# Kernel optimization log

Hardware: AMD Instinct MI355X
Metric: run time of the kernel (lower is better)

Reference implementation:

```python
import jax, jax.numpy as jnp
import numpy as np

EPS = 1e-12  # torch F.normalize eps

def _l2norm(x):
    n = jnp.linalg.norm(x, axis=-1, keepdims=True)
    return x / jnp.maximum(n, EPS)

def _encode(h, mask, W, b):
    # h: [B,S,H], mask: [B,S] int
    h = h * mask[..., None].astype(h.dtype)      # zero padded tokens
    pooled = h[:, 0]                             # pooling_type='cls'
    col = h[:, 1:] @ W + b                       # colbert_linear on tokens 1:
    return _l2norm(pooled), _l2norm(col)         # normalize=True


def setup_inputs() -> dict:
    key = jax.random.key(0)
    k1, k2, k3, k4, k5, k6 = jax.random.split(key, 6)
    Q, Sq, C, Sc, H, D = 64, 32, 256, 256, 768, 128
    return {
        "q_hidden": jax.random.normal(k1, (Q, Sq, H), jnp.float32),
        "c_hidden": jax.random.normal(k2, (C, Sc, H), jnp.float32),
        "W": jax.random.normal(k3, (H, D), jnp.float32) / np.sqrt(H).astype(np.float32),
        "b": jax.random.normal(k4, (D,), jnp.float32) * 0.01,
        "q_mask": jax.random.randint(k5, (Q, Sq), 0, 2, jnp.int32),
        "c_mask": jax.random.randint(k6, (C, Sc), 0, 2, jnp.int32),
    }


def reference(q_hidden, c_hidden, W, b, q_mask, c_mask):
    q_pooled, q_col = _encode(q_hidden, q_mask, W, b)   # q_col: [Q, Sq-1, D]
    c_pooled, c_col = _encode(c_hidden, c_mask, W, b)   # c_col: [C, Sc-1, D]
    # MaxSim late interaction (get_batch_colbert_sim)
    token_sim = jnp.einsum('qin,cjn->qicj', q_col, c_col)  # [Q, Sq-1, C, Sc-1]
    sim = token_sim.max(axis=-1)                           # max over doc tokens j
    denom = q_mask[:, 1:].sum(-1, keepdims=True).astype(sim.dtype)
    sim = sim.sum(axis=1) / denom                          # [Q, C]
    return sim, q_pooled, c_pooled
```

## Files before the change

### kernel.cpp

```cpp
#include <hip/hip_runtime.h>
#include <hip/hip_bf16.h>

#define QN 64
#define SQ 32
#define CN 256
#define SC 256
#define HD 768
#define DD 128

typedef __attribute__((ext_vector_type(8))) short short8;
typedef __attribute__((ext_vector_type(4))) float f32x4;

static __device__ __forceinline__ unsigned short f2bf(float x) {
  unsigned u = __float_as_uint(x);
  unsigned r = 0x7FFFu + ((u >> 16) & 1u);
  return (unsigned short)((u + r) >> 16);
}
static __device__ __forceinline__ unsigned pack2(float a, float b) {
  return (unsigned)f2bf(a) | ((unsigned)f2bf(b) << 16);
}

typedef const __attribute__((address_space(1))) unsigned int* as1_u32p;
typedef __attribute__((address_space(3))) unsigned int* as3_u32p;
static __device__ __forceinline__ void gl_lds16(const void* g, void* l) {
  __builtin_amdgcn_global_load_lds((as1_u32p)g, (as3_u32p)l, 16, 0, 0);
}

__global__ __launch_bounds__(256) void prep_kernel(
    const float* __restrict__ W,
    const float* __restrict__ qh, const int* __restrict__ qm,
    const float* __restrict__ ch, const int* __restrict__ cm,
    unsigned short* __restrict__ WtS,
    float* __restrict__ outq, float* __restrict__ outc,
    unsigned short* __restrict__ qcolP) {
  __shared__ float red[4];
  int bid = blockIdx.x, tid = threadIdx.x;

  if (bid < DD) {
    int d = bid;
    if (tid < 96) {
      int kc = tid;
      unsigned p[4];
#pragma unroll
      for (int e = 0; e < 4; ++e) {
        float a = W[(size_t)(kc * 8 + 2 * e) * DD + d];
        float b = W[(size_t)(kc * 8 + 2 * e + 1) * DD + d];
        p[e] = pack2(a, b);
      }
      int kcp = (kc & ~7) | ((kc & 7) ^ (d & 7));
      *(uint4*)&WtS[((size_t)d * 96 + kcp) * 8] = *(uint4*)p;
    }
    return;
  }

  int row = bid - DD;
  const float* src;
  float* dst;
  float m;
  if (row < QN) {
    src = qh + (size_t)row * SQ * HD;
    m = (float)qm[row * SQ];
    dst = outq + (size_t)row * HD;
  } else {
    int b = row - QN;
    src = ch + (size_t)b * SC * HD;
    m = (float)cm[b * SC];
    dst = outc + (size_t)b * HD;
  }
  float ss = 0.f;
  for (int k = tid; k < HD; k += 256) {
    float v = src[k] * m;
    ss += v * v;
  }
  int lane = tid & 63, wv = tid >> 6;
  for (int off = 32; off; off >>= 1) ss += __shfl_xor(ss, off);
  if (lane == 0) red[wv] = ss;
  __syncthreads();
  float tot = red[0] + red[1] + red[2] + red[3];
  float inv = 1.f / fmaxf(sqrtf(tot), 1e-12f);
  for (int k = tid; k < HD; k += 256) dst[k] = src[k] * m * inv;
  if (row < QN && tid < 64)
    ((unsigned*)(qcolP + ((size_t)row * 32 + 31) * DD))[tid] = 0u;
}

union ProjLDS {
  struct { float a[128 * 64]; unsigned short w[128 * 64]; } s;
  float cep[64 * 132];
};

__global__ __launch_bounds__(256, 3) void proj_kernel(
    const float* __restrict__ q_hidden, const float* __restrict__ c_hidden,
    const int* __restrict__ q_mask, const int* __restrict__ c_mask,
    const unsigned short* __restrict__ WtS, const float* __restrict__ bias,
    unsigned short* __restrict__ qcol, unsigned short* __restrict__ ccol) {
  __shared__ ProjLDS u;
  int bx = blockIdx.x;
  int isQ = (bx >= 510) ? 1 : 0;
  int base = isQ ? (bx - 510) : bx;
  int tid = threadIdx.x, lane = tid & 63, wv = tid >> 6;
  int lm = lane & 15, lq = lane >> 4;

  int ac = (tid & 8) | ((tid & 7) ^ ((tid >> 4) & 7));
  const float* aptr[8];
#pragma unroll
  for (int i = 0; i < 8; ++i) {
    int r = i * 16 + (tid >> 4);
    int g = base * 128 + r;
    const float* hp;
    if (isQ) {
      g = (g < 1983) ? g : 1983;
      int qq = g / 31, t = g - qq * 31;
      hp = q_hidden + ((size_t)qq * SQ + t + 1) * HD;
    } else {
      int cb = g / 255, t = g - cb * 255;
      hp = c_hidden + ((size_t)cb * SC + t + 1) * HD;
    }
    aptr[i] = hp + ac * 4;
  }
  const unsigned short* wptr[4];
#pragma unroll
  for (int i = 0; i < 4; ++i) {
    int d = i * 32 + (tid >> 3);
    wptr[i] = WtS + ((size_t)d * 96 + (tid & 7)) * 8;
  }

  f32x4 acc[2][8];
#pragma unroll
  for (int i = 0; i < 2; ++i)
#pragma unroll
    for (int j = 0; j < 8; ++j) acc[i][j] = (f32x4){0.f, 0.f, 0.f, 0.f};

  for (int step = 0; step < 12; ++step) {
    __syncthreads();
#pragma unroll
    for (int i = 0; i < 8; ++i)
      gl_lds16(aptr[i] + step * 64, (char*)u.s.a + (size_t)(i * 256 + wv * 64) * 16);
#pragma unroll
    for (int i = 0; i < 4; ++i)
      gl_lds16(wptr[i] + step * 64, (char*)u.s.w + (size_t)(i * 256 + wv * 64) * 16);
    __syncthreads();

#pragma unroll
    for (int w = 0; w < 2; ++w) {
      short8 afr[2];
#pragma unroll
      for (int mt = 0; mt < 2; ++mt) {
        int rr = wv * 32 + mt * 16 + lm;
        int x0 = (lq * 2) ^ (lm & 7);
        int x1 = (lq * 2 + 1) ^ (lm & 7);
        float4 a0 = *(const float4*)&u.s.a[rr * 64 + w * 32 + x0 * 4];
        float4 a1 = *(const float4*)&u.s.a[rr * 64 + w * 32 + x1 * 4];
        unsigned p[4];
        p[0] = pack2(a0.x, a0.y); p[1] = pack2(a0.z, a0.w);
        p[2] = pack2(a1.x, a1.y); p[3] = pack2(a1.z, a1.w);
        afr[mt] = *(short8*)p;
      }
      short8 bfr[8];
#pragma unroll
      for (int nt = 0; nt < 8; ++nt) {
        int d = nt * 16 + lm;
        int pc = (w * 4 + lq) ^ (lm & 7);
        bfr[nt] = *(const short8*)&u.s.w[d * 64 + pc * 8];
      }
#pragma unroll
      for (int mt = 0; mt < 2; ++mt)
#pragma unroll
        for (int nt = 0; nt < 8; ++nt)
          acc[mt][nt] = __builtin_amdgcn_mfma_f32_16x16x32_bf16(afr[mt], bfr[nt], acc[mt][nt], 0, 0, 0);
    }
  }

  int tk = tid >> 2, qt = tid & 3;
#pragma unroll
  for (int h = 0; h < 2; ++h) {
    __syncthreads();
    if ((wv >> 1) == h) {
#pragma unroll
      for (int mt = 0; mt < 2; ++mt)
#pragma unroll
        for (int nt = 0; nt < 8; ++nt)
#pragma unroll
          for (int r = 0; r < 4; ++r) {
            int row = (wv & 1) * 32 + mt * 16 + lq * 4 + r;
            u.cep[row * 132 + nt * 16 + lm] = acc[mt][nt][r];
          }
    }
    __syncthreads();

    int g = base * 128 + h * 64 + tk;
    int qq, t, valid = 1;
    float fm;
    if (isQ) {
      if (g > 1983) { valid = 0; g = 1983; }
      qq = g / 31; t = g - qq * 31;
      fm = (float)q_mask[qq * SQ + t + 1];
    } else {
      qq = g / 255; t = g - qq * 255;
      fm = (float)c_mask[qq * SC + t + 1];
    }

    float v[32];
    float ss = 0.f;
#pragma unroll
    for (int j = 0; j < 8; ++j) {
      float4 cv = *(const float4*)&u.cep[tk * 132 + qt * 32 + j * 4];
      float4 bv = *(const float4*)&bias[qt * 32 + j * 4];
      v[4 * j + 0] = cv.x * fm + bv.x; v[4 * j + 1] = cv.y * fm + bv.y;
      v[4 * j + 2] = cv.z * fm + bv.z; v[4 * j + 3] = cv.w * fm + bv.w;
#pragma unroll
      for (int e = 0; e < 4; ++e) ss += v[4 * j + e] * v[4 * j + e];
    }
    ss += __shfl_xor(ss, 1);
    ss += __shfl_xor(ss, 2);
    float inv = 1.f / fmaxf(sqrtf(ss), 1e-12f);

    uint4 pk4[4];
#pragma unroll
    for (int j = 0; j < 4; ++j) {
      unsigned p[4];
#pragma unroll
      for (int e = 0; e < 4; ++e)
        p[e] = pack2(v[8 * j + 2 * e] * inv, v[8 * j + 2 * e + 1] * inv);
      pk4[j] = *(uint4*)p;
    }

    if (isQ) {
      if (valid) {
        uint4* dst = (uint4*)(qcol + ((size_t)qq * 32 + t) * DD + qt * 32);
#pragma unroll
        for (int j = 0; j < 4; ++j) dst[j] = pk4[j];
      }
    } else {
      uint4* rowp = (uint4*)(ccol + ((size_t)qq * 256 + t) * DD);
#pragma unroll
      for (int j = 0; j < 4; ++j) {
        int kc = qt * 4 + j;
        int p = (kc & 8) | ((kc & 7) ^ (t & 7));
        rowp[p] = pk4[j];
      }
      if (t == 254) {
        uint4* rowp2 = rowp + 8;
#pragma unroll
        for (int j = 0; j < 4; ++j) {
          int kc = qt * 4 + j;
          int p = (kc & 8) | ((kc & 7) ^ 7);
          rowp2[p] = pk4[j];
        }
      }
    }
  }
}

__global__ __launch_bounds__(256, 2) void sim_kernel(
    const unsigned short* __restrict__ qcolP,
    const unsigned short* __restrict__ ccol,
    const int* __restrict__ qmask,
    float* __restrict__ sim) {
  __shared__ unsigned short cbuf[256 * 128];
  int tid = threadIdx.x, lane = tid & 63, wv = tid >> 6;
  int lm = lane & 15, lq = lane >> 4;
  int qb = blockIdx.y * 16 + wv * 4;
  int c0 = blockIdx.x * 2;

  short8 af[4][2][4];
#pragma unroll
  for (int q2 = 0; q2 < 4; ++q2)
#pragma unroll
    for (int it = 0; it < 2; ++it)
#pragma unroll
      for (int kf = 0; kf < 4; ++kf)
        af[q2][it][kf] = *(const short8*)(qcolP +
            (((size_t)(qb + q2) * 32 + it * 16 + lm) * DD + kf * 32 + lq * 8));

  float dinv[4];
#pragma unroll
  for (int q2 = 0; q2 < 4; ++q2) {
    float v = (lane >= 1 && lane < 32) ? (float)qmask[(qb + q2) * SQ + lane] : 0.f;
    for (int off = 1; off < 64; off <<= 1) v += __shfl_xor(v, off);
    dinv[q2] = 1.f / v;
  }

  for (int cc = 0; cc < 2; ++cc) {
    int c = c0 + cc;
    __syncthreads();
    const unsigned short* src = ccol + (size_t)c * SC * DD;
#pragma unroll
    for (int i = 0; i < 16; ++i)
      gl_lds16(src + (size_t)(i * 256 + wv * 64 + lane) * 8,
               (char*)cbuf + (size_t)(i * 256 + wv * 64) * 16);
    __syncthreads();

    float rmax[4][2];
#pragma unroll
    for (int q2 = 0; q2 < 4; ++q2) { rmax[q2][0] = -__builtin_inff(); rmax[q2][1] = -__builtin_inff(); }

    for (int jt = 0; jt < 16; ++jt) {
      short8 cf[4];
#pragma unroll
      for (int kf = 0; kf < 4; ++kf) {
        int row = jt * 16 + lm;
        int kc = kf * 4 + lq;
        int p = (kc & 8) | ((kc & 7) ^ (row & 7));
        cf[kf] = *(const short8*)&cbuf[(size_t)(row * 16 + p) * 8];
      }
#pragma unroll
      for (int q2 = 0; q2 < 4; ++q2)
#pragma unroll
        for (int it = 0; it < 2; ++it) {
          f32x4 acc = (f32x4){0.f, 0.f, 0.f, 0.f};
#pragma unroll
          for (int kf = 0; kf < 4; ++kf)
            acc = __builtin_amdgcn_mfma_f32_16x16x32_bf16(cf[kf], af[q2][it][kf], acc, 0, 0, 0);
          float loc = fmaxf(fmaxf(acc[0], acc[1]), fmaxf(acc[2], acc[3]));
          rmax[q2][it] = fmaxf(rmax[q2][it], loc);
        }
    }

#pragma unroll
    for (int q2 = 0; q2 < 4; ++q2) {
      float m0 = rmax[q2][0], m1 = rmax[q2][1];
      m0 = fmaxf(m0, __shfl_xor(m0, 16)); m0 = fmaxf(m0, __shfl_xor(m0, 32));
      m1 = fmaxf(m1, __shfl_xor(m1, 16)); m1 = fmaxf(m1, __shfl_xor(m1, 32));
      float s = m0 + ((lm == 15) ? 0.f : m1);
      s += __shfl_xor(s, 1); s += __shfl_xor(s, 2);
      s += __shfl_xor(s, 4); s += __shfl_xor(s, 8);
      if (lane == 0) sim[(qb + q2) * CN + c] = s * dinv[q2];
    }
  }
}

extern "C" void kernel_launch(void* const* d_in, const int* in_sizes, int n_in,
                              void* d_out, int out_size, void* d_ws, size_t ws_size,
                              hipStream_t stream) {
  const float* q_hidden = (const float*)d_in[0];
  const float* c_hidden = (const float*)d_in[1];
  const float* W = (const float*)d_in[2];
  const float* bias = (const float*)d_in[3];
  const int* q_mask = (const int*)d_in[4];
  const int* c_mask = (const int*)d_in[5];

  float* out = (float*)d_out;
  float* sim = out;
  float* q_pooled = out + QN * CN;
  float* c_pooled = q_pooled + QN * HD;

  unsigned short* WtS   = (unsigned short*)d_ws;
  unsigned short* qcolP = (unsigned short*)((char*)d_ws + (256 << 10));
  unsigned short* ccol  = (unsigned short*)((char*)d_ws + (1 << 20));

  prep_kernel<<<DD + QN + CN, 256, 0, stream>>>(W, q_hidden, q_mask, c_hidden, c_mask,
                                                WtS, q_pooled, c_pooled, qcolP);
  proj_kernel<<<526, 256, 0, stream>>>(q_hidden, c_hidden, q_mask, c_mask,
                                       WtS, bias, qcolP, ccol);
  sim_kernel<<<dim3(128, 4), 256, 0, stream>>>(qcolP, ccol, q_mask, sim);
}
```

Measured before the change: 362.9 us.

## Double-buffer LDS loads in projection and MaxSim kernels, halve projection tile

The projection kernel now works on 64-row tiles instead of 128-row tiles, so twice as many blocks are launched. Its K loop double-buffers the activation and weight tiles in LDS, loading the next step while MFMAs run on the current one. The MaxSim kernel splits each document's 256 tokens into two 128-row halves, also double-buffered, so global-to-LDS copies overlap compute. The projection change costs lower per-block register reuse (one M tile per wave) and occupancy drops to 2 blocks per SIMD. The pad-row write for token 255 is also corrected to land at the true next row.

```diff
diff --git a/kernel.cpp b/kernel.cpp
--- a/kernel.cpp
+++ b/kernel.cpp
@@ -84,31 +84,30 @@
 }
 
 union ProjLDS {
-  struct { float a[128 * 64]; unsigned short w[128 * 64]; } s;
+  struct { float a[2][64 * 64]; unsigned short w[2][128 * 64]; } s;
   float cep[64 * 132];
 };
 
-__global__ __launch_bounds__(256, 3) void proj_kernel(
+__global__ __launch_bounds__(256, 2) void proj_kernel(
     const float* __restrict__ q_hidden, const float* __restrict__ c_hidden,
     const int* __restrict__ q_mask, const int* __restrict__ c_mask,
     const unsigned short* __restrict__ WtS, const float* __restrict__ bias,
     unsigned short* __restrict__ qcol, unsigned short* __restrict__ ccol) {
   __shared__ ProjLDS u;
   int bx = blockIdx.x;
-  int isQ = (bx >= 510) ? 1 : 0;
-  int base = isQ ? (bx - 510) : bx;
+  int isQ = (bx >= 1020) ? 1 : 0;
+  int base = isQ ? (bx - 1020) : bx;
   int tid = threadIdx.x, lane = tid & 63, wv = tid >> 6;
   int lm = lane & 15, lq = lane >> 4;
 
   int ac = (tid & 8) | ((tid & 7) ^ ((tid >> 4) & 7));
-  const float* aptr[8];
-#pragma unroll
-  for (int i = 0; i < 8; ++i) {
+  const float* aptr[4];
+#pragma unroll
+  for (int i = 0; i < 4; ++i) {
     int r = i * 16 + (tid >> 4);
-    int g = base * 128 + r;
+    int g = base * 64 + r;
     const float* hp;
     if (isQ) {
-      g = (g < 1983) ? g : 1983;
       int qq = g / 31, t = g - qq * 31;
       hp = q_hidden + ((size_t)qq * SQ + t + 1) * HD;
     } else {
@@ -124,128 +123,118 @@
     wptr[i] = WtS + ((size_t)d * 96 + (tid & 7)) * 8;
   }
 
-  f32x4 acc[2][8];
-#pragma unroll
-  for (int i = 0; i < 2; ++i)
-#pragma unroll
-    for (int j = 0; j < 8; ++j) acc[i][j] = (f32x4){0.f, 0.f, 0.f, 0.f};
+  f32x4 acc[8];
+#pragma unroll
+  for (int j = 0; j < 8; ++j) acc[j] = (f32x4){0.f, 0.f, 0.f, 0.f};
+
+#pragma unroll
+  for (int i = 0; i < 4; ++i)
+    gl_lds16(aptr[i], (char*)&u.s.a[0][0] + (size_t)(i * 256 + wv * 64) * 16);
+#pragma unroll
+  for (int i = 0; i < 4; ++i)
+    gl_lds16(wptr[i], (char*)&u.s.w[0][0] + (size_t)(i * 256 + wv * 64) * 16);
+  __syncthreads();
 
   for (int step = 0; step < 12; ++step) {
-    __syncthreads();
-#pragma unroll
-    for (int i = 0; i < 8; ++i)
-      gl_lds16(aptr[i] + step * 64, (char*)u.s.a + (size_t)(i * 256 + wv * 64) * 16);
-#pragma unroll
-    for (int i = 0; i < 4; ++i)
-      gl_lds16(wptr[i] + step * 64, (char*)u.s.w + (size_t)(i * 256 + wv * 64) * 16);
-    __syncthreads();
-
+    int cur = step & 1;
+    if (step < 11) {
+      int nxt = cur ^ 1;
+#pragma unroll
+      for (int i = 0; i < 4; ++i)
+        gl_lds16(aptr[i] + (step + 1) * 64,
+                 (char*)&u.s.a[nxt][0] + (size_t)(i * 256 + wv * 64) * 16);
+#pragma unroll
+      for (int i = 0; i < 4; ++i)
+        gl_lds16(wptr[i] + (step + 1) * 64,
+                 (char*)&u.s.w[nxt][0] + (size_t)(i * 256 + wv * 64) * 16);
+    }
 #pragma unroll
     for (int w = 0; w < 2; ++w) {
-      short8 afr[2];
-#pragma unroll
-      for (int mt = 0; mt < 2; ++mt) {
-        int rr = wv * 32 + mt * 16 + lm;
-        int x0 = (lq * 2) ^ (lm & 7);
-        int x1 = (lq * 2 + 1) ^ (lm & 7);
-        float4 a0 = *(const float4*)&u.s.a[rr * 64 + w * 32 + x0 * 4];
-        float4 a1 = *(const float4*)&u.s.a[rr * 64 + w * 32 + x1 * 4];
-        unsigned p[4];
-        p[0] = pack2(a0.x, a0.y); p[1] = pack2(a0.z, a0.w);
-        p[2] = pack2(a1.x, a1.y); p[3] = pack2(a1.z, a1.w);
-        afr[mt] = *(short8*)p;
-      }
-      short8 bfr[8];
+      int rr = wv * 16 + lm;
+      int x0 = (lq * 2) ^ (lm & 7);
+      int x1 = (lq * 2 + 1) ^ (lm & 7);
+      float4 a0 = *(const float4*)&u.s.a[cur][rr * 64 + w * 32 + x0 * 4];
+      float4 a1 = *(const float4*)&u.s.a[cur][rr * 64 + w * 32 + x1 * 4];
+      unsigned p[4];
+      p[0] = pack2(a0.x, a0.y); p[1] = pack2(a0.z, a0.w);
+      p[2] = pack2(a1.x, a1.y); p[3] = pack2(a1.z, a1.w);
+      short8 afr = *(short8*)p;
 #pragma unroll
       for (int nt = 0; nt < 8; ++nt) {
         int d = nt * 16 + lm;
         int pc = (w * 4 + lq) ^ (lm & 7);
-        bfr[nt] = *(const short8*)&u.s.w[d * 64 + pc * 8];
-      }
-#pragma unroll
-      for (int mt = 0; mt < 2; ++mt)
-#pragma unroll
-        for (int nt = 0; nt < 8; ++nt)
-          acc[mt][nt] = __builtin_amdgcn_mfma_f32_16x16x32_bf16(afr[mt], bfr[nt], acc[mt][nt], 0, 0, 0);
-    }
-  }
+        short8 bfr = *(const short8*)&u.s.w[cur][d * 64 + pc * 8];
+        acc[nt] = __builtin_amdgcn_mfma_f32_16x16x32_bf16(afr, bfr, acc[nt], 0, 0, 0);
+      }
+    }
+    __syncthreads();
+  }
+
+#pragma unroll
+  for (int nt = 0; nt < 8; ++nt)
+#pragma unroll
+    for (int r = 0; r < 4; ++r) {
+      int row = wv * 16 + lq * 4 + r;
+      u.cep[row * 132 + nt * 16 + lm] = acc[nt][r];
+    }
+  __syncthreads();
 
   int tk = tid >> 2, qt = tid & 3;
-#pragma unroll
-  for (int h = 0; h < 2; ++h) {
-    __syncthreads();
-    if ((wv >> 1) == h) {
-#pragma unroll
-      for (int mt = 0; mt < 2; ++mt)
-#pragma unroll
-        for (int nt = 0; nt < 8; ++nt)
-#pragma unroll
-          for (int r = 0; r < 4; ++r) {
-            int row = (wv & 1) * 32 + mt * 16 + lq * 4 + r;
-            u.cep[row * 132 + nt * 16 + lm] = acc[mt][nt][r];
-          }
-    }
-    __syncthreads();
-
-    int g = base * 128 + h * 64 + tk;
-    int qq, t, valid = 1;
-    float fm;
-    if (isQ) {
-      if (g > 1983) { valid = 0; g = 1983; }
-      qq = g / 31; t = g - qq * 31;
-      fm = (float)q_mask[qq * SQ + t + 1];
-    } else {
-      qq = g / 255; t = g - qq * 255;
-      fm = (float)c_mask[qq * SC + t + 1];
-    }
-
-    float v[32];
-    float ss = 0.f;
-#pragma unroll
-    for (int j = 0; j < 8; ++j) {
-      float4 cv = *(const float4*)&u.cep[tk * 132 + qt * 32 + j * 4];
-      float4 bv = *(const float4*)&bias[qt * 32 + j * 4];
-      v[4 * j + 0] = cv.x * fm + bv.x; v[4 * j + 1] = cv.y * fm + bv.y;
-      v[4 * j + 2] = cv.z * fm + bv.z; v[4 * j + 3] = cv.w * fm + bv.w;
-#pragma unroll
-      for (int e = 0; e < 4; ++e) ss += v[4 * j + e] * v[4 * j + e];
-    }
-    ss += __shfl_xor(ss, 1);
-    ss += __shfl_xor(ss, 2);
-    float inv = 1.f / fmaxf(sqrtf(ss), 1e-12f);
-
-    uint4 pk4[4];
+  int g = base * 64 + tk;
+  int qq, t;
+  float fm;
+  if (isQ) {
+    qq = g / 31; t = g - qq * 31;
+    fm = (float)q_mask[qq * SQ + t + 1];
+  } else {
+    qq = g / 255; t = g - qq * 255;
+    fm = (float)c_mask[qq * SC + t + 1];
+  }
+
+  float v[32];
+  float ss = 0.f;
+#pragma unroll
+  for (int j = 0; j < 8; ++j) {
+    float4 cv = *(const float4*)&u.cep[tk * 132 + qt * 32 + j * 4];
+    float4 bv = *(const float4*)&bias[qt * 32 + j * 4];
+    v[4 * j + 0] = cv.x * fm + bv.x; v[4 * j + 1] = cv.y * fm + bv.y;
+    v[4 * j + 2] = cv.z * fm + bv.z; v[4 * j + 3] = cv.w * fm + bv.w;
+#pragma unroll
+    for (int e = 0; e < 4; ++e) ss += v[4 * j + e] * v[4 * j + e];
+  }
+  ss += __shfl_xor(ss, 1);
+  ss += __shfl_xor(ss, 2);
+  float inv = 1.f / fmaxf(sqrtf(ss), 1e-12f);
+
+  uint4 pk4[4];
+#pragma unroll
+  for (int j = 0; j < 4; ++j) {
+    unsigned p[4];
+#pragma unroll
+    for (int e = 0; e < 4; ++e)
+      p[e] = pack2(v[8 * j + 2 * e] * inv, v[8 * j + 2 * e + 1] * inv);
+    pk4[j] = *(uint4*)p;
+  }
+
+  if (isQ) {
+    uint4* dst = (uint4*)(qcol + ((size_t)qq * 32 + t) * DD + qt * 32);
+#pragma unroll
+    for (int j = 0; j < 4; ++j) dst[j] = pk4[j];
+  } else {
+    uint4* rowp = (uint4*)(ccol + ((size_t)qq * 256 + t) * DD);
 #pragma unroll
     for (int j = 0; j < 4; ++j) {
-      unsigned p[4];
-#pragma unroll
-      for (int e = 0; e < 4; ++e)
-        p[e] = pack2(v[8 * j + 2 * e] * inv, v[8 * j + 2 * e + 1] * inv);
-      pk4[j] = *(uint4*)p;
-    }
-
-    if (isQ) {
-      if (valid) {
-        uint4* dst = (uint4*)(qcol + ((size_t)qq * 32 + t) * DD + qt * 32);
-#pragma unroll
-        for (int j = 0; j < 4; ++j) dst[j] = pk4[j];
-      }
-    } else {
-      uint4* rowp = (uint4*)(ccol + ((size_t)qq * 256 + t) * DD);
+      int kc = qt * 4 + j;
+      int p = (kc & 8) | ((kc & 7) ^ (t & 7));
+      rowp[p] = pk4[j];
+    }
+    if (t == 254) {
+      uint4* rowp2 = rowp + 16;
 #pragma unroll
       for (int j = 0; j < 4; ++j) {
         int kc = qt * 4 + j;
-        int p = (kc & 8) | ((kc & 7) ^ (t & 7));
-        rowp[p] = pk4[j];
-      }
-      if (t == 254) {
-        uint4* rowp2 = rowp + 8;
-#pragma unroll
-        for (int j = 0; j < 4; ++j) {
-          int kc = qt * 4 + j;
-          int p = (kc & 8) | ((kc & 7) ^ 7);
-          rowp2[p] = pk4[j];
-        }
+        int p = (kc & 8) | ((kc & 7) ^ 7);
+        rowp2[p] = pk4[j];
       }
     }
   }
@@ -256,7 +245,7 @@
     const unsigned short* __restrict__ ccol,
     const int* __restrict__ qmask,
     float* __restrict__ sim) {
-  __shared__ unsigned short cbuf[256 * 128];
+  __shared__ unsigned short cbuf[2][128 * 128];
   int tid = threadIdx.x, lane = tid & 63, wv = tid >> 6;
   int lm = lane & 15, lq = lane >> 4;
   int qb = blockIdx.y * 16 + wv * 4;
@@ -280,28 +269,40 @@
     dinv[q2] = 1.f / v;
   }
 
-  for (int cc = 0; cc < 2; ++cc) {
-    int c = c0 + cc;
-    __syncthreads();
-    const unsigned short* src = ccol + (size_t)c * SC * DD;
-#pragma unroll
-    for (int i = 0; i < 16; ++i)
-      gl_lds16(src + (size_t)(i * 256 + wv * 64 + lane) * 8,
-               (char*)cbuf + (size_t)(i * 256 + wv * 64) * 16);
-    __syncthreads();
-
-    float rmax[4][2];
-#pragma unroll
-    for (int q2 = 0; q2 < 4; ++q2) { rmax[q2][0] = -__builtin_inff(); rmax[q2][1] = -__builtin_inff(); }
-
-    for (int jt = 0; jt < 16; ++jt) {
+  const unsigned short* csrc = ccol + (size_t)c0 * SC * DD;
+
+#pragma unroll
+  for (int i = 0; i < 8; ++i)
+    gl_lds16(csrc + (size_t)(i * 256 + tid) * 8,
+             (char*)&cbuf[0][0] + (size_t)(i * 256 + wv * 64) * 16);
+  __syncthreads();
+
+  float rmax[4][2];
+  for (int ht = 0; ht < 4; ++ht) {
+    int b = ht & 1;
+    if (!(ht & 1)) {
+#pragma unroll
+      for (int q2 = 0; q2 < 4; ++q2) {
+        rmax[q2][0] = -__builtin_inff();
+        rmax[q2][1] = -__builtin_inff();
+      }
+    }
+    if (ht < 3) {
+      const unsigned short* s2 = csrc + (size_t)(ht + 1) * 16384;
+#pragma unroll
+      for (int i = 0; i < 8; ++i)
+        gl_lds16(s2 + (size_t)(i * 256 + tid) * 8,
+                 (char*)&cbuf[b ^ 1][0] + (size_t)(i * 256 + wv * 64) * 16);
+    }
+
+    for (int jt = 0; jt < 8; ++jt) {
       short8 cf[4];
 #pragma unroll
       for (int kf = 0; kf < 4; ++kf) {
         int row = jt * 16 + lm;
         int kc = kf * 4 + lq;
         int p = (kc & 8) | ((kc & 7) ^ (row & 7));
-        cf[kf] = *(const short8*)&cbuf[(size_t)(row * 16 + p) * 8];
+        cf[kf] = *(const short8*)&cbuf[b][(size_t)(row * 16 + p) * 8];
       }
 #pragma unroll
       for (int q2 = 0; q2 < 4; ++q2)
@@ -316,16 +317,20 @@
         }
     }
 
-#pragma unroll
-    for (int q2 = 0; q2 < 4; ++q2) {
-      float m0 = rmax[q2][0], m1 = rmax[q2][1];
-      m0 = fmaxf(m0, __shfl_xor(m0, 16)); m0 = fmaxf(m0, __shfl_xor(m0, 32));
-      m1 = fmaxf(m1, __shfl_xor(m1, 16)); m1 = fmaxf(m1, __shfl_xor(m1, 32));
-      float s = m0 + ((lm == 15) ? 0.f : m1);
-      s += __shfl_xor(s, 1); s += __shfl_xor(s, 2);
-      s += __shfl_xor(s, 4); s += __shfl_xor(s, 8);
-      if (lane == 0) sim[(qb + q2) * CN + c] = s * dinv[q2];
-    }
+    if (ht & 1) {
+      int c = c0 + (ht >> 1);
+#pragma unroll
+      for (int q2 = 0; q2 < 4; ++q2) {
+        float m0 = rmax[q2][0], m1 = rmax[q2][1];
+        m0 = fmaxf(m0, __shfl_xor(m0, 16)); m0 = fmaxf(m0, __shfl_xor(m0, 32));
+        m1 = fmaxf(m1, __shfl_xor(m1, 16)); m1 = fmaxf(m1, __shfl_xor(m1, 32));
+        float s = m0 + ((lm == 15) ? 0.f : m1);
+        s += __shfl_xor(s, 1); s += __shfl_xor(s, 2);
+        s += __shfl_xor(s, 4); s += __shfl_xor(s, 8);
+        if (lane == 0) sim[(qb + q2) * CN + c] = s * dinv[q2];
+      }
+    }
+    __syncthreads();
   }
 }
 
@@ -350,7 +355,7 @@
 
   prep_kernel<<<DD + QN + CN, 256, 0, stream>>>(W, q_hidden, q_mask, c_hidden, c_mask,
                                                 WtS, q_pooled, c_pooled, qcolP);
-  proj_kernel<<<526, 256, 0, stream>>>(q_hidden, c_hidden, q_mask, c_mask,
-                                       WtS, bias, qcolP, ccol);
+  proj_kernel<<<1051, 256, 0, stream>>>(q_hidden, c_hidden, q_mask, c_mask,
+                                        WtS, bias, qcolP, ccol);
   sim_kernel<<<dim3(128, 4), 256, 0, stream>>>(qcolP, ccol, q_mask, sim);
 }
```

New measurement: 361.3 us. Within noise of the previous version (-0.4%).
